# Performance work log

Hardware: AMD Instinct MI355X
Metric: run time of the kernel (lower is better)

## Reference

```python
import jax, jax.numpy as jnp
import numpy as np

HIDDEN = 2048
NUM_HEADS = 32
NUM_KV_HEADS = 8
GROUP = NUM_HEADS // NUM_KV_HEADS  # 4
HEAD_DIM = HIDDEN // NUM_HEADS     # 64
SEQ = 2048


def setup_inputs() -> dict:
    key = jax.random.key(0)
    ks = jax.random.split(key, 5)
    s = HIDDEN ** -0.5
    x = jax.random.normal(ks[0], (SEQ, HIDDEN), jnp.float32)
    q_proj = jax.random.normal(ks[1], (HIDDEN, HIDDEN), jnp.float32) * s
    k_proj = jax.random.normal(ks[2], (HIDDEN, HIDDEN // GROUP), jnp.float32) * s
    v_proj = jax.random.normal(ks[3], (HIDDEN, HIDDEN // GROUP), jnp.float32) * s
    o_proj = jax.random.normal(ks[4], (HIDDEN, HIDDEN), jnp.float32) * s
    # inv_freq = 1/rsqrt(10000**(i/d)) = sqrt(10000**(i/d)) per the original module
    inv_freq = jnp.sqrt(10000.0 ** (jnp.arange(0, HEAD_DIM, 2) / HEAD_DIM)).astype(jnp.float32)
    return {"x": x, "q_proj": q_proj, "k_proj": k_proj, "v_proj": v_proj,
            "o_proj": o_proj, "inv_freq": inv_freq}


def _rope(x, inv_freq):
    # x: [S, ..., HEAD_DIM]; rotation per the original (nonstandard) formula.
    orig_dtype = x.dtype
    x = x.astype(jnp.float32)
    seq = jnp.arange(x.shape[0])
    angles = seq[:, None] * jax.lax.stop_gradient(inv_freq)[None, :]  # [S, HEAD_DIM//2]
    bshape = (x.shape[0],) + (1,) * (x.ndim - 2) + (HEAD_DIM // 2,)
    sins = jnp.sin(angles).reshape(bshape)
    coss = jnp.cos(angles).reshape(bshape)
    half, odd = jnp.split(x, 2, axis=-1)
    out = jnp.concatenate([half * coss + odd * sins, half * sins - odd * coss], axis=-1)
    return out.astype(orig_dtype)


def reference(x, q_proj, k_proj, v_proj, o_proj, inv_freq):
    S = x.shape[0]
    q = (x @ q_proj).reshape(S, NUM_KV_HEADS, GROUP, HEAD_DIM)
    k = (x @ k_proj).reshape(S, NUM_KV_HEADS, HEAD_DIM)
    v = (x @ v_proj).reshape(S, NUM_KV_HEADS, HEAD_DIM)
    q = _rope(q, inv_freq)
    k = _rope(k, inv_freq)
    # scores: [a=S, b=S, h=kv_heads, g=group]
    scores = jnp.einsum('ahgd,bhd->abhg', q, k) / (HEAD_DIM ** 0.5)
    mask = jnp.tril(jnp.ones((S, S), dtype=jnp.bool_))[:, :, None, None]
    scores = jnp.where(mask, scores, -jnp.inf)
    attn = jax.nn.softmax(scores, axis=1)  # softmax over b (axis=-3)
    o = jnp.einsum('abhg,bhd->ahgd', attn, v).reshape(S, HIDDEN)
    return o @ o_proj
```

## Files before the change

kernel.cpp:

```cpp
#include <hip/hip_runtime.h>


typedef __bf16 bf16_t;
typedef __bf16 bf16x4 __attribute__((ext_vector_type(4)));
typedef __bf16 bf16x8 __attribute__((ext_vector_type(8)));
typedef float  f32x4  __attribute__((ext_vector_type(4)));
typedef short  s16x4  __attribute__((ext_vector_type(4)));

#define S_LEN   2048
#define HID     2048
#define NKV     8
#define NH      32
#define DHEAD   64
#define KVW     (NKV * DHEAD)

__device__ __align__(16) bf16_t g_xb [S_LEN * HID];
__device__ __align__(16) bf16_t g_wTq[HID * HID];
__device__ __align__(16) bf16_t g_wTk[KVW * HID];
__device__ __align__(16) bf16_t g_wTv[KVW * HID];
__device__ __align__(16) bf16_t g_wTo[HID * HID];
__device__ __align__(16) bf16_t g_q [S_LEN * HID];
__device__ __align__(16) bf16_t g_k [S_LEN * KVW];
__device__ __align__(16) bf16_t g_vT[KVW * S_LEN];
__device__ __align__(16) bf16_t g_om[S_LEN * HID];
__device__ float g_ropeC[S_LEN * 32];
__device__ float g_ropeS[S_LEN * 32];
__device__ __align__(16) float g_po[4u * S_LEN * HID];
__device__ float g_pl[4u * S_LEN * NH];

static __device__ inline s16x4 bc4(bf16x4 v) { s16x4 r; __builtin_memcpy(&r, &v, 8); return r; }

__device__ __forceinline__ void gll16(void* lds, const void* g) {
    __builtin_amdgcn_global_load_lds(
        (const __attribute__((address_space(1))) void*)g,
        (__attribute__((address_space(3))) void*)lds,
        16, 0, 0);
}

__global__ __launch_bounds__(256)
void prep_kernel(const float* __restrict__ x,
                 const float* __restrict__ qw, const float* __restrict__ kw,
                 const float* __restrict__ vw, const float* __restrict__ ow,
                 const void* __restrict__ invf_raw) {
    __shared__ bf16_t tile[64][65];
    int b = blockIdx.x, t = threadIdx.x;

    if (b < 256) {
        int idx = b * 256 + t;
        int s = idx >> 5, j = idx & 31;
        float f;
        if (*(const unsigned*)invf_raw == 0x3F800000u) {
            f = ((const float*)invf_raw)[j];
        } else {
            unsigned u = ((unsigned)((const unsigned short*)invf_raw)[j]) << 16;
            __builtin_memcpy(&f, &u, 4);
        }
        double a = (double)s * (double)f;
        g_ropeC[idx] = (float)cos(a);
        g_ropeS[idx] = (float)sin(a);
        return;
    }
    if (b < 4352) {
        int idx = (b - 256) * 256 + t;
        float4 v = reinterpret_cast<const float4*>(x)[idx];
        bf16x4 o;
        o[0] = (bf16_t)v.x; o[1] = (bf16_t)v.y; o[2] = (bf16_t)v.z; o[3] = (bf16_t)v.w;
        *reinterpret_cast<bf16x4*>(&g_xb[(size_t)idx * 4]) = o;
        return;
    }
    const float* in; bf16_t* outp; int R, C, tb;
    if (b < 5376)      { in = qw; outp = g_wTq; R = HID; C = HID; tb = b - 4352; }
    else if (b < 5632) { in = kw; outp = g_wTk; R = HID; C = KVW; tb = b - 5376; }
    else if (b < 5888) { in = vw; outp = g_wTv; R = HID; C = KVW; tb = b - 5632; }
    else               { in = ow; outp = g_wTo; R = HID; C = HID; tb = b - 5888; }
    int xt = C >> 6;
    int c0 = (tb % xt) * 64, r0 = (tb / xt) * 64;
    int tx = t & 63, ty = t >> 6;
    #pragma unroll
    for (int r = ty; r < 64; r += 4)
        tile[r][tx] = (bf16_t)in[(size_t)(r0 + r) * C + c0 + tx];
    __syncthreads();
    #pragma unroll
    for (int r = ty; r < 64; r += 4)
        outp[(size_t)(c0 + r) * R + r0 + tx] = tile[tx][r];
}

__global__ __launch_bounds__(256)
void gemm_fused_kernel(float* __restrict__ Cf, int which) {
    __shared__ __align__(16) bf16_t As[2][128 * 64];
    __shared__ __align__(16) bf16_t Bs[2][128 * 64];

    int t    = threadIdx.x;
    int lane = t & 63, wid = t >> 6;
    int quad = lane >> 4, l15 = lane & 15;
    int bx = blockIdx.x, m0 = blockIdx.y * 128;
    int wm = (wid >> 1) * 64, wn = (wid & 1) * 64;

    const bf16_t* A; const bf16_t* Bt; int n0;
    if (which == 1)      { A = g_om; Bt = g_wTo; n0 = bx * 128; }
    else {
        A = g_xb;
        if (bx < 16)      { Bt = g_wTq; n0 = bx * 128; }
        else if (bx < 20) { Bt = g_wTk; n0 = (bx - 16) * 128; }
        else              { Bt = g_wTv; n0 = (bx - 20) * 128; }
    }

    int crow = lane >> 3;
    int gseg = (lane & 7) ^ crow;
    int so   = l15 & 7;

    f32x4 acc[4][4];
    #pragma unroll
    for (int im = 0; im < 4; ++im)
        #pragma unroll
        for (int in = 0; in < 4; ++in)
            #pragma unroll
            for (int r = 0; r < 4; ++r) acc[im][in][r] = 0.f;

    auto stage = [&](int buf, int kt) {
        int c0 = wid * 4;
        #pragma unroll
        for (int c = 0; c < 4; ++c) {
            gll16(&As[buf][(c0 + c) * 512],
                  A  + (size_t)(m0 + (c0 + c) * 8 + crow) * HID + kt + gseg * 8);
            gll16(&Bs[buf][(c0 + c) * 512],
                  Bt + (size_t)(n0 + (c0 + c) * 8 + crow) * HID + kt + gseg * 8);
        }
    };

    stage(0, 0);

    for (int it = 0; it < 32; ++it) {
        int cur = it & 1;
        if (it + 1 < 32) {
            stage(cur ^ 1, (it + 1) * 64);
            asm volatile("s_waitcnt vmcnt(8)" ::: "memory");
        } else {
            asm volatile("s_waitcnt vmcnt(0)" ::: "memory");
        }
        asm volatile("s_barrier" ::: "memory");

        #pragma unroll
        for (int kh = 0; kh < 2; ++kh) {
            bf16x8 af[4], bfv[4];
            #pragma unroll
            for (int i = 0; i < 4; ++i) {
                af[i]  = *reinterpret_cast<const bf16x8*>(
                    &As[cur][(wm + i * 16 + l15) * 64 + (((kh * 4 + quad) ^ so) * 8)]);
                bfv[i] = *reinterpret_cast<const bf16x8*>(
                    &Bs[cur][(wn + i * 16 + l15) * 64 + (((kh * 4 + quad) ^ so) * 8)]);
            }
            #pragma unroll
            for (int im = 0; im < 4; ++im)
                #pragma unroll
                for (int in = 0; in < 4; ++in)
                    acc[im][in] = __builtin_amdgcn_mfma_f32_16x16x32_bf16(
                        af[im], bfv[in], acc[im][in], 0, 0, 0);
        }

        asm volatile("s_barrier" ::: "memory");
    }

    if (which == 1) {
        #pragma unroll
        for (int im = 0; im < 4; ++im) {
            int rowb = m0 + wm + im * 16 + quad * 4;
            #pragma unroll
            for (int in = 0; in < 4; ++in) {
                int col = bx * 128 + wn + in * 16 + l15;
                #pragma unroll
                for (int r = 0; r < 4; ++r)
                    Cf[(size_t)(rowb + r) * HID + col] = acc[im][in][r];
            }
        }
    } else if (bx < 20) {
        bf16_t* Cb; int N, colbase;
        if (bx < 16) { Cb = g_q; N = HID; colbase = bx * 128 + wn; }
        else         { Cb = g_k; N = KVW; colbase = (bx - 16) * 128 + wn; }
        #pragma unroll
        for (int im = 0; im < 4; ++im) {
            #pragma unroll
            for (int r = 0; r < 4; ++r) {
                int row = m0 + wm + im * 16 + quad * 4 + r;
                #pragma unroll
                for (int in = 0; in < 2; ++in) {
                    int d = in * 16 + l15;
                    float a  = acc[im][in][r];
                    float bb = acc[im][in + 2][r];
                    float cc = g_ropeC[row * 32 + d];
                    float ss = g_ropeS[row * 32 + d];
                    Cb[(size_t)row * N + colbase + d]      = (bf16_t)(a * cc + bb * ss);
                    Cb[(size_t)row * N + colbase + 32 + d] = (bf16_t)(a * ss - bb * cc);
                }
            }
        }
    } else {
        #pragma unroll
        for (int im = 0; im < 4; ++im) {
            int rowb = m0 + wm + im * 16 + quad * 4;
            #pragma unroll
            for (int in = 0; in < 4; ++in) {
                int col = (bx - 20) * 128 + wn + in * 16 + l15;
                #pragma unroll
                for (int r = 0; r < 4; ++r)
                    g_vT[(size_t)col * S_LEN + (rowb + r)] = (bf16_t)acc[im][in][r];
            }
        }
    }
}

__global__ __launch_bounds__(256)
void flash_part_kernel() {
    __shared__ __align__(16) bf16_t Ks[64][72];
    __shared__ __align__(16) bf16_t Vs[64][72];

    int t    = threadIdx.x;
    int lane = t & 63, wid = t >> 6;
    int quad = lane >> 4, l15 = lane & 15;
    int bx   = blockIdx.x;
    int hk   = bx & 7;
    int qb32 = (bx >> 3) & 63;
    int chunk = bx >> 9;
    int nkt  = (qb32 >> 1) + 1;
    int kt0  = chunk * 8;
    if (kt0 >= nkt) return;
    int kt1  = min(kt0 + 8, nkt);

    int head = hk * 4 + wid;
    int q0   = qb32 * 32;

    bf16x8 aq[2][2];
    #pragma unroll
    for (int mq = 0; mq < 2; ++mq) {
        const bf16_t* qp = g_q + (size_t)(q0 + mq * 16 + l15) * HID + head * 64 + quad * 8;
        aq[mq][0] = *reinterpret_cast<const bf16x8*>(qp);
        aq[mq][1] = *reinterpret_cast<const bf16x8*>(qp + 32);
        #pragma unroll
        for (int j = 0; j < 8; ++j) {
            aq[mq][0][j] = (bf16_t)((float)aq[mq][0][j] * 0.125f);
            aq[mq][1][j] = (bf16_t)((float)aq[mq][1][j] * 0.125f);
        }
    }

    bf16x4 ones4;
    #pragma unroll
    for (int j = 0; j < 4; ++j) ones4[j] = (bf16_t)1.0f;
    s16x4 ones_s = bc4(ones4);

    f32x4 oacc[2][4], liacc[2];
    #pragma unroll
    for (int mq = 0; mq < 2; ++mq) {
        #pragma unroll
        for (int r = 0; r < 4; ++r) liacc[mq][r] = 0.f;
        #pragma unroll
        for (int dt = 0; dt < 4; ++dt)
            #pragma unroll
            for (int r = 0; r < 4; ++r) oacc[mq][dt][r] = 0.f;
    }

    int qcol[2] = { q0 + l15, q0 + 16 + l15 };

    for (int kt = kt0; kt < kt1; ++kt) {
        int k0 = kt * 64;
        __syncthreads();
        #pragma unroll
        for (int i = t; i < 512; i += 256) {
            int row = i >> 3, seg = i & 7;
            *reinterpret_cast<int4*>(&Ks[row][seg * 8]) =
                *reinterpret_cast<const int4*>(g_k + (size_t)(k0 + row) * KVW + hk * 64 + seg * 8);
            *reinterpret_cast<int4*>(&Vs[row][seg * 8]) =
                *reinterpret_cast<const int4*>(g_vT + (size_t)(hk * 64 + row) * S_LEN + k0 + seg * 8);
        }
        __syncthreads();

        bf16x8 ak[4][2];
        #pragma unroll
        for (int mk = 0; mk < 4; ++mk) {
            ak[mk][0] = *reinterpret_cast<const bf16x8*>(&Ks[mk * 16 + l15][quad * 8]);
            ak[mk][1] = *reinterpret_cast<const bf16x8*>(&Ks[mk * 16 + l15][32 + quad * 8]);
        }

        f32x4 sacc[4][2];
        #pragma unroll
        for (int mk = 0; mk < 4; ++mk)
            #pragma unroll
            for (int mq = 0; mq < 2; ++mq) {
                f32x4 s;
                #pragma unroll
                for (int r = 0; r < 4; ++r) s[r] = 0.f;
                s = __builtin_amdgcn_mfma_f32_16x16x32_bf16(ak[mk][0], aq[mq][0], s, 0, 0, 0);
                s = __builtin_amdgcn_mfma_f32_16x16x32_bf16(ak[mk][1], aq[mq][1], s, 0, 0, 0);
                sacc[mk][mq] = s;
            }

        s16x4 pas[4][2];
        #pragma unroll
        for (int mk = 0; mk < 4; ++mk)
            #pragma unroll
            for (int mq = 0; mq < 2; ++mq) {
                bf16x4 pa;
                #pragma unroll
                for (int r = 0; r < 4; ++r) {
                    int kk = k0 + mk * 16 + quad * 4 + r;
                    pa[r] = (bf16_t)((kk <= qcol[mq]) ? __expf(sacc[mk][mq][r] - 16.0f) : 0.0f);
                }
                pas[mk][mq] = bc4(pa);
            }

        #pragma unroll
        for (int mk = 0; mk < 4; ++mk) {
            #pragma unroll
            for (int dt = 0; dt < 4; ++dt) {
                bf16x4 bv = *reinterpret_cast<const bf16x4*>(&Vs[dt * 16 + l15][mk * 16 + quad * 4]);
                s16x4 bvs = bc4(bv);
                #pragma unroll
                for (int mq = 0; mq < 2; ++mq)
                    oacc[mq][dt] = __builtin_amdgcn_mfma_f32_16x16x16bf16_1k(pas[mk][mq], bvs, oacc[mq][dt], 0, 0, 0);
            }
            #pragma unroll
            for (int mq = 0; mq < 2; ++mq)
                liacc[mq] = __builtin_amdgcn_mfma_f32_16x16x16bf16_1k(pas[mk][mq], ones_s, liacc[mq], 0, 0, 0);
        }
    }

    float* po = g_po + (size_t)chunk * S_LEN * HID;
    #pragma unroll
    for (int mq = 0; mq < 2; ++mq)
        #pragma unroll
        for (int r = 0; r < 4; ++r) {
            int row = q0 + mq * 16 + quad * 4 + r;
            #pragma unroll
            for (int dt = 0; dt < 4; ++dt)
                po[(size_t)row * HID + head * 64 + dt * 16 + l15] = oacc[mq][dt][r];
            if (l15 == 0)
                g_pl[((size_t)chunk * S_LEN + row) * NH + head] = liacc[mq][r];
        }
}

__global__ __launch_bounds__(256)
void flash_combine_kernel() {
    int t = blockIdx.x * 256 + threadIdx.x;
    int row  = t >> 9;
    int col4 = (t & 511) * 4;
    int head = col4 >> 6;
    int nkt  = ((row >> 5) >> 1) + 1;
    int nc   = (nkt + 7) >> 3;

    float4 s = make_float4(0.f, 0.f, 0.f, 0.f);
    float l = 0.f;
    for (int c = 0; c < nc; ++c) {
        const float4 v = *reinterpret_cast<const float4*>(
            g_po + ((size_t)c * S_LEN + row) * HID + col4);
        s.x += v.x; s.y += v.y; s.z += v.z; s.w += v.w;
        l += g_pl[((size_t)c * S_LEN + row) * NH + head];
    }
    float inv = 1.0f / l;
    bf16x4 o;
    o[0] = (bf16_t)(s.x * inv); o[1] = (bf16_t)(s.y * inv);
    o[2] = (bf16_t)(s.z * inv); o[3] = (bf16_t)(s.w * inv);
    *reinterpret_cast<bf16x4*>(&g_om[(size_t)row * HID + col4]) = o;
}

extern "C" void kernel_launch(void* const* d_in, const int* in_sizes, int n_in,
                              void* d_out, int out_size, void* d_ws, size_t ws_size,
                              hipStream_t stream) {
    const float* x    = (const float*)d_in[0];
    const float* qpW  = (const float*)d_in[1];
    const float* kpW  = (const float*)d_in[2];
    const float* vpW  = (const float*)d_in[3];
    const float* opW  = (const float*)d_in[4];
    const void*  invf = d_in[5];
    float* out = (float*)d_out;

    prep_kernel<<<6912, 256, 0, stream>>>(x, qpW, kpW, vpW, opW, invf);
    gemm_fused_kernel<<<dim3(24, 16), 256, 0, stream>>>(nullptr, 0);
    flash_part_kernel<<<2048, 256, 0, stream>>>();
    flash_combine_kernel<<<4096, 256, 0, stream>>>();
    gemm_fused_kernel<<<dim3(16, 16), 256, 0, stream>>>(out, 1);
}
```

Before: 257.0 us.

## Shrink GEMM tiles to 128x64 with XCD-aware block remap; flash loads K/V directly

The GEMM kernel moves from 128x128 to 128x64 output tiles. This doubles the block count (768 and 512 blocks) to fill more CUs, and a 1D grid is remapped so blocks that are consecutive across the 8 XCDs share A/B panels in L2. The RoPE epilogue is adapted to 64-wide head tiles. The flash kernel drops its shared-memory staging of K and V and the two barriers, reading MFMA fragments straight from global/L2 instead, at the cost of less coalesced, redundant per-wave global loads.

```diff
diff --git a/kernel.cpp b/kernel.cpp
--- a/kernel.cpp
+++ b/kernel.cpp
@@ -88,44 +88,51 @@
 __global__ __launch_bounds__(256)
 void gemm_fused_kernel(float* __restrict__ Cf, int which) {
     __shared__ __align__(16) bf16_t As[2][128 * 64];
-    __shared__ __align__(16) bf16_t Bs[2][128 * 64];
+    __shared__ __align__(16) bf16_t Bs[2][64 * 64];
 
     int t    = threadIdx.x;
     int lane = t & 63, wid = t >> 6;
     int quad = lane >> 4, l15 = lane & 15;
-    int bx = blockIdx.x, m0 = blockIdx.y * 128;
-    int wm = (wid >> 1) * 64, wn = (wid & 1) * 64;
+
+    int ntn  = (which == 1) ? 32 : 48;
+    int nwg  = ntn * 16;
+    int orig = blockIdx.x;
+    int qq   = nwg >> 3;
+    int wg   = (orig & 7) * qq + (orig >> 3);
+    int my   = wg / ntn, nx = wg - my * ntn;
+    int m0   = my * 128;
 
     const bf16_t* A; const bf16_t* Bt; int n0;
-    if (which == 1)      { A = g_om; Bt = g_wTo; n0 = bx * 128; }
+    if (which == 1)      { A = g_om; Bt = g_wTo; n0 = nx * 64; }
     else {
         A = g_xb;
-        if (bx < 16)      { Bt = g_wTq; n0 = bx * 128; }
-        else if (bx < 20) { Bt = g_wTk; n0 = (bx - 16) * 128; }
-        else              { Bt = g_wTv; n0 = (bx - 20) * 128; }
+        if (nx < 32)      { Bt = g_wTq; n0 = nx * 64; }
+        else if (nx < 40) { Bt = g_wTk; n0 = (nx - 32) * 64; }
+        else              { Bt = g_wTv; n0 = (nx - 40) * 64; }
     }
 
     int crow = lane >> 3;
     int gseg = (lane & 7) ^ crow;
     int so   = l15 & 7;
-
-    f32x4 acc[4][4];
-    #pragma unroll
-    for (int im = 0; im < 4; ++im)
+    int wm   = wid * 32;
+
+    f32x4 acc[2][4];
+    #pragma unroll
+    for (int im = 0; im < 2; ++im)
         #pragma unroll
         for (int in = 0; in < 4; ++in)
             #pragma unroll
             for (int r = 0; r < 4; ++r) acc[im][in][r] = 0.f;
 
     auto stage = [&](int buf, int kt) {
-        int c0 = wid * 4;
-        #pragma unroll
-        for (int c = 0; c < 4; ++c) {
-            gll16(&As[buf][(c0 + c) * 512],
-                  A  + (size_t)(m0 + (c0 + c) * 8 + crow) * HID + kt + gseg * 8);
-            gll16(&Bs[buf][(c0 + c) * 512],
-                  Bt + (size_t)(n0 + (c0 + c) * 8 + crow) * HID + kt + gseg * 8);
-        }
+        #pragma unroll
+        for (int c = 0; c < 4; ++c)
+            gll16(&As[buf][(wid * 4 + c) * 512],
+                  A  + (size_t)(m0 + (wid * 4 + c) * 8 + crow) * HID + kt + gseg * 8);
+        #pragma unroll
+        for (int c = 0; c < 2; ++c)
+            gll16(&Bs[buf][(wid * 2 + c) * 512],
+                  Bt + (size_t)(n0 + (wid * 2 + c) * 8 + crow) * HID + kt + gseg * 8);
     };
 
     stage(0, 0);
@@ -134,7 +141,7 @@
         int cur = it & 1;
         if (it + 1 < 32) {
             stage(cur ^ 1, (it + 1) * 64);
-            asm volatile("s_waitcnt vmcnt(8)" ::: "memory");
+            asm volatile("s_waitcnt vmcnt(6)" ::: "memory");
         } else {
             asm volatile("s_waitcnt vmcnt(0)" ::: "memory");
         }
@@ -142,16 +149,17 @@
 
         #pragma unroll
         for (int kh = 0; kh < 2; ++kh) {
-            bf16x8 af[4], bfv[4];
-            #pragma unroll
-            for (int i = 0; i < 4; ++i) {
+            bf16x8 af[2], bfv[4];
+            #pragma unroll
+            for (int i = 0; i < 2; ++i)
                 af[i]  = *reinterpret_cast<const bf16x8*>(
                     &As[cur][(wm + i * 16 + l15) * 64 + (((kh * 4 + quad) ^ so) * 8)]);
+            #pragma unroll
+            for (int i = 0; i < 4; ++i)
                 bfv[i] = *reinterpret_cast<const bf16x8*>(
-                    &Bs[cur][(wn + i * 16 + l15) * 64 + (((kh * 4 + quad) ^ so) * 8)]);
-            }
-            #pragma unroll
-            for (int im = 0; im < 4; ++im)
+                    &Bs[cur][(i * 16 + l15) * 64 + (((kh * 4 + quad) ^ so) * 8)]);
+            #pragma unroll
+            for (int im = 0; im < 2; ++im)
                 #pragma unroll
                 for (int in = 0; in < 4; ++in)
                     acc[im][in] = __builtin_amdgcn_mfma_f32_16x16x32_bf16(
@@ -163,22 +171,22 @@
 
     if (which == 1) {
         #pragma unroll
-        for (int im = 0; im < 4; ++im) {
+        for (int im = 0; im < 2; ++im) {
             int rowb = m0 + wm + im * 16 + quad * 4;
             #pragma unroll
             for (int in = 0; in < 4; ++in) {
-                int col = bx * 128 + wn + in * 16 + l15;
+                int col = n0 + in * 16 + l15;
                 #pragma unroll
                 for (int r = 0; r < 4; ++r)
                     Cf[(size_t)(rowb + r) * HID + col] = acc[im][in][r];
             }
         }
-    } else if (bx < 20) {
+    } else if (nx < 40) {
         bf16_t* Cb; int N, colbase;
-        if (bx < 16) { Cb = g_q; N = HID; colbase = bx * 128 + wn; }
-        else         { Cb = g_k; N = KVW; colbase = (bx - 16) * 128 + wn; }
-        #pragma unroll
-        for (int im = 0; im < 4; ++im) {
+        if (nx < 32) { Cb = g_q; N = HID; colbase = nx * 64; }
+        else         { Cb = g_k; N = KVW; colbase = (nx - 32) * 64; }
+        #pragma unroll
+        for (int im = 0; im < 2; ++im) {
             #pragma unroll
             for (int r = 0; r < 4; ++r) {
                 int row = m0 + wm + im * 16 + quad * 4 + r;
@@ -196,11 +204,11 @@
         }
     } else {
         #pragma unroll
-        for (int im = 0; im < 4; ++im) {
+        for (int im = 0; im < 2; ++im) {
             int rowb = m0 + wm + im * 16 + quad * 4;
             #pragma unroll
             for (int in = 0; in < 4; ++in) {
-                int col = (bx - 20) * 128 + wn + in * 16 + l15;
+                int col = (nx - 40) * 64 + in * 16 + l15;
                 #pragma unroll
                 for (int r = 0; r < 4; ++r)
                     g_vT[(size_t)col * S_LEN + (rowb + r)] = (bf16_t)acc[im][in][r];
@@ -211,9 +219,6 @@
 
 __global__ __launch_bounds__(256)
 void flash_part_kernel() {
-    __shared__ __align__(16) bf16_t Ks[64][72];
-    __shared__ __align__(16) bf16_t Vs[64][72];
-
     int t    = threadIdx.x;
     int lane = t & 63, wid = t >> 6;
     int quad = lane >> 4, l15 = lane & 15;
@@ -262,22 +267,13 @@
 
     for (int kt = kt0; kt < kt1; ++kt) {
         int k0 = kt * 64;
-        __syncthreads();
-        #pragma unroll
-        for (int i = t; i < 512; i += 256) {
-            int row = i >> 3, seg = i & 7;
-            *reinterpret_cast<int4*>(&Ks[row][seg * 8]) =
-                *reinterpret_cast<const int4*>(g_k + (size_t)(k0 + row) * KVW + hk * 64 + seg * 8);
-            *reinterpret_cast<int4*>(&Vs[row][seg * 8]) =
-                *reinterpret_cast<const int4*>(g_vT + (size_t)(hk * 64 + row) * S_LEN + k0 + seg * 8);
-        }
-        __syncthreads();
 
         bf16x8 ak[4][2];
         #pragma unroll
         for (int mk = 0; mk < 4; ++mk) {
-            ak[mk][0] = *reinterpret_cast<const bf16x8*>(&Ks[mk * 16 + l15][quad * 8]);
-            ak[mk][1] = *reinterpret_cast<const bf16x8*>(&Ks[mk * 16 + l15][32 + quad * 8]);
+            const bf16_t* kp = g_k + (size_t)(k0 + mk * 16 + l15) * KVW + hk * 64 + quad * 8;
+            ak[mk][0] = *reinterpret_cast<const bf16x8*>(kp);
+            ak[mk][1] = *reinterpret_cast<const bf16x8*>(kp + 32);
         }
 
         f32x4 sacc[4][2];
@@ -311,7 +307,8 @@
         for (int mk = 0; mk < 4; ++mk) {
             #pragma unroll
             for (int dt = 0; dt < 4; ++dt) {
-                bf16x4 bv = *reinterpret_cast<const bf16x4*>(&Vs[dt * 16 + l15][mk * 16 + quad * 4]);
+                bf16x4 bv = *reinterpret_cast<const bf16x4*>(
+                    g_vT + (size_t)(hk * 64 + dt * 16 + l15) * S_LEN + k0 + mk * 16 + quad * 4);
                 s16x4 bvs = bc4(bv);
                 #pragma unroll
                 for (int mq = 0; mq < 2; ++mq)
@@ -373,8 +370,8 @@
     float* out = (float*)d_out;
 
     prep_kernel<<<6912, 256, 0, stream>>>(x, qpW, kpW, vpW, opW, invf);
-    gemm_fused_kernel<<<dim3(24, 16), 256, 0, stream>>>(nullptr, 0);
+    gemm_fused_kernel<<<768, 256, 0, stream>>>(nullptr, 0);
     flash_part_kernel<<<2048, 256, 0, stream>>>();
     flash_combine_kernel<<<4096, 256, 0, stream>>>();
-    gemm_fused_kernel<<<dim3(16, 16), 256, 0, stream>>>(out, 1);
-}
+    gemm_fused_kernel<<<512, 256, 0, stream>>>(out, 1);
+}
```

New measurement: 326.9 us. 1.27x slower.
